# Optimization experiments

Measured on AMD Instinct MI355X. Metric: run time of the kernel, lower is better.

## Reference

```python
import jax, jax.numpy as jnp
import numpy as np

N, T, D, H, K = 2048, 128, 256, 256, 12
MAX_ITER = 100  # k-means max_iter from _cluster default


def setup_inputs() -> dict:
    key = jax.random.key(0)
    ks = jax.random.split(key, 16)
    std = 1.0 / np.sqrt(H).astype(np.float32)
    u = lambda k, shape: jax.random.uniform(k, shape, jnp.float32, -std, std)
    return {
        "x": jax.random.normal(ks[0], (N, T, D), jnp.float32),
        "lengths": jax.random.randint(ks[1], (N,), 1, T + 1),  # valid lens in [1, T]
        # GRU params (PyTorch layout: [3H, in], gate order r,z,n)
        "W_ih": u(ks[2], (3 * H, D)),
        "W_hh": u(ks[3], (3 * H, H)),
        "b_ih": u(ks[4], (3 * H,)),
        "b_hh": u(ks[5], (3 * H,)),
        # weight1 / weight2: nn.Linear(H, 1)
        "w1_w": u(ks[6], (1, H)), "w1_b": u(ks[7], (1,)),
        "w2_w": u(ks[8], (1, H)), "w2_b": u(ks[9], (1,)),
        # GCN layers: weight [H, H], bias [H]
        "g1_w": u(ks[10], (H, H)), "g1_b": u(ks[11], (H,)),
        "g2_w": u(ks[12], (H, H)), "g2_b": u(ks[13], (H,)),
    }


def _gru(x, W_ih, W_hh, b_ih, b_hh):
    # x: [N, T, D] -> outputs [T, N, H]
    def step(h, x_t):
        gx = x_t @ W_ih.T + b_ih          # [N, 3H]
        gh = h @ W_hh.T + b_hh            # [N, 3H]
        xr, xz, xn = jnp.split(gx, 3, axis=-1)
        hr, hz, hn = jnp.split(gh, 3, axis=-1)
        r = jax.nn.sigmoid(xr + hr)
        z = jax.nn.sigmoid(xz + hz)
        n = jnp.tanh(xn + r * hn)
        h_new = (1.0 - z) * n + z * h
        return h_new, h_new

    h0 = jnp.zeros((x.shape[0], W_hh.shape[1]), x.dtype)
    _, outs = jax.lax.scan(step, h0, jnp.swapaxes(x, 0, 1))
    return outs  # [T, N, H]


def _kmeans(data, k, max_iter=MAX_ITER):
    # data: [n, H]. Fixed-iteration Lloyd's: after convergence centers are a
    # fixed point, so running all max_iter iters matches the early-break loop.
    n = data.shape[0]
    idx = jax.random.permutation(jax.random.key(42), n)[:k]  # random init
    centers0 = data[idx]
    x2 = jnp.sum(data * data, axis=1, keepdims=True)  # [n, 1]

    def body(_, centers):
        # squared distances (same argmin as cdist)
        d2 = x2 - 2.0 * (data @ centers.T) + jnp.sum(centers * centers, axis=1)
        codes = jnp.argmin(d2, axis=1)  # [n]
        sums = jax.ops.segment_sum(data, codes, num_segments=k)       # [k, H]
        cnts = jax.ops.segment_sum(jnp.ones((n,), data.dtype), codes, num_segments=k)
        # empty clusters keep old center
        return jnp.where(cnts[:, None] > 0,
                         sums / jnp.maximum(cnts[:, None], 1.0),
                         centers)

    return jax.lax.fori_loop(0, max_iter, body, centers0)


def reference(x, lengths, W_ih, W_hh, b_ih, b_hh,
              w1_w, w1_b, w2_w, w2_b, g1_w, g1_b, g2_w, g2_b):
    outs = _gru(x, W_ih, W_hh, b_ih, b_hh)              # [T, N, H]
    n = x.shape[0]
    hidden_t = outs[lengths - 1, jnp.arange(n)]         # last valid step, [N, H]

    # clustering uses detached hidden states
    centers = _kmeans(jax.lax.stop_gradient(hidden_t), K)  # [K, H]

    e = jax.nn.relu(hidden_t @ centers.T)               # [N, K]
    scores = jax.nn.softmax(e, axis=-1)

    # adj = eye(K) so GraphConvolution reduces to an affine map
    h1 = jax.nn.relu(centers @ g1_w + g1_b)             # [K, H]
    h2 = jax.nn.relu(h1 @ g2_w + g2_b)                  # [K, H]

    clu_app = scores @ h2                               # [N, H]
    w1 = jax.nn.sigmoid(clu_app @ w1_w.T + w1_b)        # [N, 1]
    w2 = jax.nn.sigmoid(hidden_t @ w2_w.T + w2_b)       # [N, 1]
    w1n = w1 / (w1 + w2)
    return w1n * clu_app + (1.0 - w1n) * hidden_t       # [N, H]
```

## Files before the change

kernel.cpp:

```cpp
#include <hip/hip_runtime.h>
#include <cstdint>
#include <cstring>
#include <vector>
#include <algorithm>


namespace {
constexpr int Nn = 2048;
constexpr int Tt = 128;
constexpr int Dd = 256;
constexpr int Hh = 256;
constexpr int Kk = 12;
constexpr int MAXIT = 100;
}

struct IdxArgs { int v[Kk]; };

typedef float v2f __attribute__((ext_vector_type(2)));

__device__ __forceinline__ float sigm(float x) { return 1.0f / (1.0f + expf(-x)); }

#define PKFMA(A, X, W) \
  asm("v_pk_fma_f32 %0, %1, %2, %0" : "+v"(A) : "v"(X), "v"(W))
#define LO2(V) ((v2f){(V).x, (V).y})
#define HI2(V) ((v2f){(V).z, (V).w})

__global__ __launch_bounds__(64) void pack_w(
    const float* __restrict__ Wih, const float* __restrict__ Whh,
    float* __restrict__ pk)
{
  const int j = blockIdx.x;
  const int k4 = threadIdx.x;
  const int g = j >> 8, c = j & 255;
  float4 vih = *(const float4*)&Wih[(size_t)j * 256 + k4 * 4];
  float4 vhh = *(const float4*)&Whh[(size_t)j * 256 + k4 * 4];
  *(float4*)&pk[(((size_t)k4 * 6 + g) * 256 + c) * 4]       = vih;
  *(float4*)&pk[(((size_t)k4 * 6 + 3 + g) * 256 + c) * 4]   = vhh;
}

__global__ __launch_bounds__(512, 1) void gru_q(
    const float* __restrict__ x, const int* __restrict__ len,
    const float* __restrict__ pk,
    const float* __restrict__ bih, const float* __restrict__ bhh,
    float* __restrict__ hfin)
{
  __shared__ alignas(16) float xls[8][260];
  __shared__ alignas(16) float hls[8][260];
  __shared__ float4 pbuf[2][8][256];
  const int tid = threadIdx.x;
  const int cp = tid & 127;
  const int q  = tid >> 7;
  const int n0 = blockIdx.x * 8;
  const int C0 = cp, C1 = cp + 128;

  const float bir0 = bih[C0], bhr0 = bhh[C0];
  const float biz0 = bih[Hh + C0], bhz0 = bhh[Hh + C0];
  const float bin0 = bih[2 * Hh + C0], bhn0 = bhh[2 * Hh + C0];
  const float bir1 = bih[C1], bhr1 = bhh[C1];
  const float biz1 = bih[Hh + C1], bhz1 = bhh[Hh + C1];
  const float bin1 = bih[2 * Hh + C1], bhn1 = bhh[2 * Hh + C1];
  int L[8];
  #pragma unroll
  for (int r = 0; r < 8; ++r) L[r] = len[n0 + r];

  const int q16 = q * 16;
  const size_t cp4 = (size_t)cp * 4;

  if (tid < 256) {
    #pragma unroll
    for (int r = 0; r < 8; ++r) hls[r][tid] = 0.f;
  }

  for (int t = 0; t < Tt; ++t) {
    {
      int row = tid >> 6, c4 = tid & 63;
      *(float4*)&xls[row][c4 * 4] =
          *(const float4*)&x[(size_t)(n0 + row) * (Tt * Dd) + (size_t)t * Dd + c4 * 4];
    }
    __syncthreads();

    v2f aR[8][2] = {}, aZ[8][2] = {}, aXN[8][2] = {}, aHN[8][2] = {};

    #pragma unroll 1
    for (int i = 0; i < 16; ++i) {
      const int k4 = q16 + i;
      const float* pb = pk + (size_t)k4 * 6144 + cp4;
      float4 wr0 = *(const float4*)(pb);
      float4 wr1 = *(const float4*)(pb + 512);
      float4 wz0 = *(const float4*)(pb + 1024);
      float4 wz1 = *(const float4*)(pb + 1536);
      float4 wn0 = *(const float4*)(pb + 2048);
      float4 wn1 = *(const float4*)(pb + 2560);
      const int k = k4 * 4;
      #pragma unroll
      for (int r = 0; r < 8; ++r) {
        float4 xv = *(const float4*)&xls[r][k];
        v2f xlo = LO2(xv), xhi = HI2(xv);
        PKFMA(aR[r][0],  xlo, LO2(wr0)); PKFMA(aR[r][0],  xhi, HI2(wr0));
        PKFMA(aR[r][1],  xlo, LO2(wr1)); PKFMA(aR[r][1],  xhi, HI2(wr1));
        PKFMA(aZ[r][0],  xlo, LO2(wz0)); PKFMA(aZ[r][0],  xhi, HI2(wz0));
        PKFMA(aZ[r][1],  xlo, LO2(wz1)); PKFMA(aZ[r][1],  xhi, HI2(wz1));
        PKFMA(aXN[r][0], xlo, LO2(wn0)); PKFMA(aXN[r][0], xhi, HI2(wn0));
        PKFMA(aXN[r][1], xlo, LO2(wn1)); PKFMA(aXN[r][1], xhi, HI2(wn1));
      }
    }
    #pragma unroll 1
    for (int i = 0; i < 16; ++i) {
      const int k4 = q16 + i;
      const float* pb = pk + (size_t)k4 * 6144 + 3072 + cp4;
      float4 wr0 = *(const float4*)(pb);
      float4 wr1 = *(const float4*)(pb + 512);
      float4 wz0 = *(const float4*)(pb + 1024);
      float4 wz1 = *(const float4*)(pb + 1536);
      float4 wn0 = *(const float4*)(pb + 2048);
      float4 wn1 = *(const float4*)(pb + 2560);
      const int k = k4 * 4;
      #pragma unroll
      for (int r = 0; r < 8; ++r) {
        float4 hv = *(const float4*)&hls[r][k];
        v2f hlo = LO2(hv), hhi = HI2(hv);
        PKFMA(aR[r][0],  hlo, LO2(wr0)); PKFMA(aR[r][0],  hhi, HI2(wr0));
        PKFMA(aR[r][1],  hlo, LO2(wr1)); PKFMA(aR[r][1],  hhi, HI2(wr1));
        PKFMA(aZ[r][0],  hlo, LO2(wz0)); PKFMA(aZ[r][0],  hhi, HI2(wz0));
        PKFMA(aZ[r][1],  hlo, LO2(wz1)); PKFMA(aZ[r][1],  hhi, HI2(wz1));
        PKFMA(aHN[r][0], hlo, LO2(wn0)); PKFMA(aHN[r][0], hhi, HI2(wn0));
        PKFMA(aHN[r][1], hlo, LO2(wn1)); PKFMA(aHN[r][1], hhi, HI2(wn1));
      }
    }

    float fR[8][2], fZ[8][2], fX[8][2], fH[8][2];
    #pragma unroll
    for (int r = 0; r < 8; ++r) {
      fR[r][0] = aR[r][0].x + aR[r][0].y;  fR[r][1] = aR[r][1].x + aR[r][1].y;
      fZ[r][0] = aZ[r][0].x + aZ[r][0].y;  fZ[r][1] = aZ[r][1].x + aZ[r][1].y;
      fX[r][0] = aXN[r][0].x + aXN[r][0].y; fX[r][1] = aXN[r][1].x + aXN[r][1].y;
      fH[r][0] = aHN[r][0].x + aHN[r][0].y; fH[r][1] = aHN[r][1].x + aHN[r][1].y;
    }

    if (q == 1 || q == 3) {
      const int reg = q >> 1;
      #pragma unroll
      for (int r = 0; r < 8; ++r) {
        pbuf[reg][r][C0] = make_float4(fR[r][0], fZ[r][0], fX[r][0], fH[r][0]);
        pbuf[reg][r][C1] = make_float4(fR[r][1], fZ[r][1], fX[r][1], fH[r][1]);
      }
    }
    __syncthreads();
    if (q == 0 || q == 2) {
      const int reg = q >> 1;
      #pragma unroll
      for (int r = 0; r < 8; ++r) {
        float4 p0 = pbuf[reg][r][C0];
        float4 p1 = pbuf[reg][r][C1];
        fR[r][0] += p0.x; fZ[r][0] += p0.y; fX[r][0] += p0.z; fH[r][0] += p0.w;
        fR[r][1] += p1.x; fZ[r][1] += p1.y; fX[r][1] += p1.z; fH[r][1] += p1.w;
      }
    }
    __syncthreads();
    if (q == 2) {
      #pragma unroll
      for (int r = 0; r < 8; ++r) {
        pbuf[0][r][C0] = make_float4(fR[r][0], fZ[r][0], fX[r][0], fH[r][0]);
        pbuf[0][r][C1] = make_float4(fR[r][1], fZ[r][1], fX[r][1], fH[r][1]);
      }
    }
    __syncthreads();

    if (q == 0) {
      #pragma unroll
      for (int r = 0; r < 8; ++r) {
        if (t < L[r]) {
          float4 p0 = pbuf[0][r][C0];
          float4 p1 = pbuf[0][r][C1];
          float sR0 = fR[r][0] + p0.x, sZ0 = fZ[r][0] + p0.y;
          float sX0 = fX[r][0] + p0.z, sH0 = fH[r][0] + p0.w;
          float sR1 = fR[r][1] + p1.x, sZ1 = fZ[r][1] + p1.y;
          float sX1 = fX[r][1] + p1.z, sH1 = fH[r][1] + p1.w;
          float rg0 = sigm(sR0 + bir0 + bhr0);
          float zg0 = sigm(sZ0 + biz0 + bhz0);
          float ng0 = tanhf(sX0 + bin0 + rg0 * (sH0 + bhn0));
          float hv0 = (1.f - zg0) * ng0 + zg0 * hls[r][C0];
          float rg1 = sigm(sR1 + bir1 + bhr1);
          float zg1 = sigm(sZ1 + biz1 + bhz1);
          float ng1 = tanhf(sX1 + bin1 + rg1 * (sH1 + bhn1));
          float hv1 = (1.f - zg1) * ng1 + zg1 * hls[r][C1];
          hls[r][C0] = hv0;
          hls[r][C1] = hv1;
          if (t == L[r] - 1) {
            hfin[(size_t)(n0 + r) * Hh + C0] = hv0;
            hfin[(size_t)(n0 + r) * Hh + C1] = hv1;
          }
        }
      }
    }
    __syncthreads();
  }
}

__global__ void km_init(const float* __restrict__ dat, float* __restrict__ cent,
                        int* __restrict__ codes_prev, IdxArgs ia)
{
  int c = threadIdx.x;
  #pragma unroll
  for (int k = 0; k < Kk; ++k)
    cent[k * Hh + c] = dat[(size_t)ia.v[k] * Hh + c];
  #pragma unroll
  for (int i = 0; i < 8; ++i) codes_prev[i * 256 + c] = -1;
}

__global__ __launch_bounds__(256) void km_assign(
    const float* __restrict__ dat, const float* __restrict__ cent,
    float* __restrict__ part, int* __restrict__ pcnt,
    int* __restrict__ codes_prev, int* __restrict__ chg_it,
    const int* __restrict__ done)
{
  if (done[0]) return;
  __shared__ alignas(16) float cs[Kk][Hh];
  __shared__ alignas(16) float ps[4][Kk][Hh];
  __shared__ float c2s[Kk];
  __shared__ int pc[4][Kk];
  __shared__ int chg_l;
  const int tid = threadIdx.x;
  const int lane = tid & 63;
  const int w = tid >> 6;

  for (int i = tid; i < Kk * Hh; i += 256) ((float*)cs)[i] = cent[i];
  for (int i = tid; i < 4 * Kk * Hh; i += 256) ((float*)ps)[i] = 0.f;
  if (tid < 4 * Kk) ((int*)pc)[tid] = 0;
  if (tid == 0) chg_l = 0;
  __syncthreads();
  if (tid < Kk) {
    float s = 0.f;
    for (int c = 0; c < Hh; ++c) { float v = cs[tid][c]; s += v * v; }
    c2s[tid] = s;
  }
  __syncthreads();

  int mych = 0;
  const int base = blockIdx.x * 64 + w * 16;
  for (int rr = 0; rr < 16; ++rr) {
    const int n = base + rr;
    float4 v = *(const float4*)&dat[(size_t)n * Hh + lane * 4];
    float best = 3.4e38f; int bi = 0;
    #pragma unroll
    for (int k = 0; k < Kk; ++k) {
      float4 cv = *(const float4*)&cs[k][lane * 4];
      float p = v.x * cv.x + v.y * cv.y + v.z * cv.z + v.w * cv.w;
      #pragma unroll
      for (int m = 1; m < 64; m <<= 1) p += __shfl_xor(p, m, 64);
      float d = c2s[k] - 2.f * p;
      if (d < best) { best = d; bi = k; }
    }
    float4* dst = (float4*)&ps[w][bi][lane * 4];
    float4 cur = *dst;
    cur.x += v.x; cur.y += v.y; cur.z += v.z; cur.w += v.w;
    *dst = cur;
    if (lane == 0) {
      pc[w][bi] += 1;
      if (codes_prev[n] != bi) { codes_prev[n] = bi; mych = 1; }
    }
  }
  if (mych) atomicOr(&chg_l, 1);
  __syncthreads();
  const float* p0 = &ps[0][0][0];
  for (int i = tid; i < Kk * Hh; i += 256)
    part[(size_t)blockIdx.x * (Kk * Hh) + i] =
        p0[i] + p0[Kk * Hh + i] + p0[2 * Kk * Hh + i] + p0[3 * Kk * Hh + i];
  if (tid < Kk)
    pcnt[blockIdx.x * Kk + tid] = pc[0][tid] + pc[1][tid] + pc[2][tid] + pc[3][tid];
  if (tid == 0 && chg_l) atomicOr(chg_it, 1);
}

__global__ __launch_bounds__(256) void km_update(
    const float* __restrict__ part, const int* __restrict__ pcnt,
    float* __restrict__ cent, const int* __restrict__ chg_it,
    int* __restrict__ done)
{
  if (done[0]) return;
  int k = blockIdx.x, c = threadIdx.x;
  int cnt = 0;
  for (int p = 0; p < 32; ++p) cnt += pcnt[p * Kk + k];
  float s = 0.f;
  for (int p = 0; p < 32; ++p) s += part[(size_t)p * (Kk * Hh) + k * Hh + c];
  if (cnt > 0) cent[k * Hh + c] = s / (float)cnt;
  if (k == 0 && c == 0 && chg_it[0] == 0) done[0] = 1;
}

__global__ __launch_bounds__(256) void gcn(
    const float* __restrict__ cent, const float* __restrict__ g1w,
    const float* __restrict__ g1b, const float* __restrict__ g2w,
    const float* __restrict__ g2b, float* __restrict__ h2out)
{
  __shared__ float a[Kk][Hh];
  __shared__ float b[Kk][Hh];
  int c = threadIdx.x;
  for (int i = c; i < Kk * Hh; i += 256) ((float*)a)[i] = cent[i];
  __syncthreads();
  float acc[Kk];
  #pragma unroll
  for (int k = 0; k < Kk; ++k) acc[k] = 0.f;
  for (int j = 0; j < Hh; ++j) {
    float wv = g1w[(size_t)j * Hh + c];
    #pragma unroll
    for (int k = 0; k < Kk; ++k) acc[k] += a[k][j] * wv;
  }
  #pragma unroll
  for (int k = 0; k < Kk; ++k) b[k][c] = fmaxf(acc[k] + g1b[c], 0.f);
  __syncthreads();
  #pragma unroll
  for (int k = 0; k < Kk; ++k) acc[k] = 0.f;
  for (int j = 0; j < Hh; ++j) {
    float wv = g2w[(size_t)j * Hh + c];
    #pragma unroll
    for (int k = 0; k < Kk; ++k) acc[k] += b[k][j] * wv;
  }
  #pragma unroll
  for (int k = 0; k < Kk; ++k) h2out[k * Hh + c] = fmaxf(acc[k] + g2b[c], 0.f);
}

__global__ __launch_bounds__(256) void finalk(
    const float* __restrict__ hfin, const float* __restrict__ cent,
    const float* __restrict__ h2, const float* __restrict__ w1w,
    const float* __restrict__ w1b, const float* __restrict__ w2w,
    const float* __restrict__ w2b, float* __restrict__ out)
{
  __shared__ alignas(16) float cs[Kk][Hh];
  __shared__ alignas(16) float hs[Kk][Hh];
  __shared__ float red[4];
  const int tid = threadIdx.x, lane = tid & 63, w = tid >> 6;
  const int n = blockIdx.x;
  for (int i = tid; i < Kk * Hh; i += 256) { ((float*)cs)[i] = cent[i]; ((float*)hs)[i] = h2[i]; }
  float ht = hfin[(size_t)n * Hh + tid];
  __syncthreads();

  auto bred = [&](float v) -> float {
    #pragma unroll
    for (int m = 1; m < 64; m <<= 1) v += __shfl_xor(v, m, 64);
    __syncthreads();
    if (lane == 0) red[w] = v;
    __syncthreads();
    return red[0] + red[1] + red[2] + red[3];
  };

  float ev[Kk];
  #pragma unroll
  for (int k = 0; k < Kk; ++k)
    ev[k] = fmaxf(bred(ht * cs[k][tid]), 0.f);

  float mx = ev[0];
  #pragma unroll
  for (int k = 1; k < Kk; ++k) mx = fmaxf(mx, ev[k]);
  float se = 0.f; float sc[Kk];
  #pragma unroll
  for (int k = 0; k < Kk; ++k) { sc[k] = expf(ev[k] - mx); se += sc[k]; }
  float inv = 1.f / se;
  float clu = 0.f;
  #pragma unroll
  for (int k = 0; k < Kk; ++k) clu += sc[k] * inv * hs[k][tid];

  float r1 = bred(clu * w1w[tid]);
  float r2 = bred(ht * w2w[tid]);
  float a1 = sigm(r1 + w1b[0]);
  float a2 = sigm(r2 + w2b[0]);
  float wn = a1 / (a1 + a2);
  out[(size_t)n * Hh + tid] = wn * clu + (1.f - wn) * ht;
}

static void tf2x32(uint32_t k0, uint32_t k1, uint32_t c0, uint32_t c1,
                   uint32_t& o0, uint32_t& o1) {
  uint32_t ks2 = k0 ^ k1 ^ 0x1BD11BDAu;
  uint32_t x0 = c0 + k0, x1 = c1 + k1;
#define TFR(r) do { x0 += x1; x1 = (x1 << (r)) | (x1 >> (32 - (r))); x1 ^= x0; } while (0)
  TFR(13); TFR(15); TFR(26); TFR(6);
  x0 += k1;  x1 += ks2 + 1u;
  TFR(17); TFR(29); TFR(16); TFR(24);
  x0 += ks2; x1 += k0 + 2u;
  TFR(13); TFR(15); TFR(26); TFR(6);
  x0 += k0;  x1 += k1 + 3u;
  TFR(17); TFR(29); TFR(16); TFR(24);
  x0 += k1;  x1 += ks2 + 4u;
  TFR(13); TFR(15); TFR(26); TFR(6);
  x0 += ks2; x1 += k0 + 5u;
#undef TFR
  o0 = x0; o1 = x1;
}

static void compute_idx(int* out12) {
  uint32_t kh = 0u, kl = 42u;
  std::vector<int> perm(Nn);
  for (int i = 0; i < Nn; ++i) perm[i] = i;
  std::vector<uint32_t> bits(Nn);
  std::vector<int> pos(Nn);
  for (int round = 0; round < 2; ++round) {
    uint32_t nh, nl, sh, sl;
    tf2x32(kh, kl, 0u, 0u, nh, nl);
    tf2x32(kh, kl, 0u, 1u, sh, sl);
    kh = nh; kl = nl;
    for (uint32_t i = 0; i < (uint32_t)Nn; ++i) {
      uint32_t o0, o1; tf2x32(sh, sl, 0u, i, o0, o1); bits[i] = o0 ^ o1;
    }
    for (int i = 0; i < Nn; ++i) pos[i] = i;
    std::stable_sort(pos.begin(), pos.end(),
                     [&](int a, int b) { return bits[a] < bits[b]; });
    std::vector<int> np(Nn);
    for (int i = 0; i < Nn; ++i) np[i] = perm[pos[i]];
    perm.swap(np);
  }
  for (int k = 0; k < Kk; ++k) out12[k] = perm[k];
}

extern "C" void kernel_launch(void* const* d_in, const int* in_sizes, int n_in,
                              void* d_out, int out_size, void* d_ws, size_t ws_size,
                              hipStream_t stream) {
  const float* x   = (const float*)d_in[0];
  const int*   len = (const int*)d_in[1];
  const float* Wih = (const float*)d_in[2];
  const float* Whh = (const float*)d_in[3];
  const float* bih = (const float*)d_in[4];
  const float* bhh = (const float*)d_in[5];
  const float* w1w = (const float*)d_in[6];
  const float* w1b = (const float*)d_in[7];
  const float* w2w = (const float*)d_in[8];
  const float* w2b = (const float*)d_in[9];
  const float* g1w = (const float*)d_in[10];
  const float* g1b = (const float*)d_in[11];
  const float* g2w = (const float*)d_in[12];
  const float* g2b = (const float*)d_in[13];
  float* out = (float*)d_out;

  float* wsf  = (float*)d_ws;
  float* hfin = wsf;
  float* cent = hfin + (size_t)Nn * Hh;
  float* h2g  = cent + Kk * Hh;
  float* part = h2g + Kk * Hh;
  int*   pcnt = (int*)(part + 32 * Kk * Hh);
  int*   codes = pcnt + 512;
  int*   chg  = codes + Nn;
  float* pkw  = (float*)(chg + MAXIT + 28);

  IdxArgs ia;
  compute_idx(ia.v);

  hipMemsetAsync(chg, 0, (MAXIT + 1) * sizeof(int), stream);
  pack_w<<<768, 64, 0, stream>>>(Wih, Whh, pkw);
  gru_q<<<256, 512, 0, stream>>>(x, len, pkw, bih, bhh, hfin);

  int* done = chg + MAXIT;
  km_init<<<1, 256, 0, stream>>>(hfin, cent, codes, ia);
  for (int it = 0; it < MAXIT; ++it) {
    km_assign<<<32, 256, 0, stream>>>(hfin, cent, part, pcnt, codes, chg + it, done);
    km_update<<<Kk, 256, 0, stream>>>(part, pcnt, cent, chg + it, done);
  }

  gcn<<<1, 256, 0, stream>>>(cent, g1w, g1b, g2w, g2b, h2g);
  finalk<<<Nn, 256, 0, stream>>>(hfin, cent, h2g, w1w, w1b, w2w, w2b, out);
}
```

Measured before the change: 4.664 ms.

## Fuse k-means centroid update into assignment kernel with double-buffered partials

```diff
diff --git a/kernel.cpp b/kernel.cpp
--- a/kernel.cpp
+++ b/kernel.cpp
@@ -208,13 +208,18 @@
   for (int i = 0; i < 8; ++i) codes_prev[i * 256 + c] = -1;
 }
 
-__global__ __launch_bounds__(256) void km_assign(
-    const float* __restrict__ dat, const float* __restrict__ cent,
-    float* __restrict__ part, int* __restrict__ pcnt,
-    int* __restrict__ codes_prev, int* __restrict__ chg_it,
-    const int* __restrict__ done)
+__global__ __launch_bounds__(256) void km_step(
+    const float* __restrict__ dat, float* __restrict__ cent,
+    float* __restrict__ partA, float* __restrict__ partB,
+    int* __restrict__ pcntA, int* __restrict__ pcntB,
+    int* __restrict__ codes_prev, int* __restrict__ chg,
+    int* __restrict__ done, int it)
 {
   if (done[0]) return;
+  if (it > 0 && chg[it - 1] == 0) {
+    if (blockIdx.x == 0 && threadIdx.x == 0) done[0] = 1;
+    return;
+  }
   __shared__ alignas(16) float cs[Kk][Hh];
   __shared__ alignas(16) float ps[4][Kk][Hh];
   __shared__ float c2s[Kk];
@@ -223,12 +228,31 @@
   const int tid = threadIdx.x;
   const int lane = tid & 63;
   const int w = tid >> 6;
-
-  for (int i = tid; i < Kk * Hh; i += 256) ((float*)cs)[i] = cent[i];
+  float* pw = (it & 1) ? partB : partA;
+  const float* pr = (it & 1) ? partA : partB;
+  int* cw = (it & 1) ? pcntB : pcntA;
+  const int* cr = (it & 1) ? pcntA : pcntB;
+
+  if (it == 0) {
+    for (int i = tid; i < Kk * Hh; i += 256) ((float*)cs)[i] = cent[i];
+  } else {
+    const int c = tid;
+    #pragma unroll
+    for (int k = 0; k < Kk; ++k) {
+      int cnt = 0;
+      for (int p = 0; p < 32; ++p) cnt += cr[p * Kk + k];
+      float s = 0.f;
+      for (int p = 0; p < 32; ++p) s += pr[(size_t)p * (Kk * Hh) + k * Hh + c];
+      cs[k][c] = (cnt > 0) ? s / (float)cnt : cent[k * Hh + c];
+    }
+  }
   for (int i = tid; i < 4 * Kk * Hh; i += 256) ((float*)ps)[i] = 0.f;
   if (tid < 4 * Kk) ((int*)pc)[tid] = 0;
   if (tid == 0) chg_l = 0;
   __syncthreads();
+  if (it > 0 && blockIdx.x == 0) {
+    for (int i = tid; i < Kk * Hh; i += 256) cent[i] = ((const float*)cs)[i];
+  }
   if (tid < Kk) {
     float s = 0.f;
     for (int c = 0; c < Hh; ++c) { float v = cs[tid][c]; s += v * v; }
@@ -264,26 +288,24 @@
   __syncthreads();
   const float* p0 = &ps[0][0][0];
   for (int i = tid; i < Kk * Hh; i += 256)
-    part[(size_t)blockIdx.x * (Kk * Hh) + i] =
+    pw[(size_t)blockIdx.x * (Kk * Hh) + i] =
         p0[i] + p0[Kk * Hh + i] + p0[2 * Kk * Hh + i] + p0[3 * Kk * Hh + i];
   if (tid < Kk)
-    pcnt[blockIdx.x * Kk + tid] = pc[0][tid] + pc[1][tid] + pc[2][tid] + pc[3][tid];
-  if (tid == 0 && chg_l) atomicOr(chg_it, 1);
-}
-
-__global__ __launch_bounds__(256) void km_update(
-    const float* __restrict__ part, const int* __restrict__ pcnt,
-    float* __restrict__ cent, const int* __restrict__ chg_it,
-    int* __restrict__ done)
+    cw[blockIdx.x * Kk + tid] = pc[0][tid] + pc[1][tid] + pc[2][tid] + pc[3][tid];
+  if (tid == 0 && chg_l) atomicOr(chg + it, 1);
+}
+
+__global__ __launch_bounds__(256) void km_final(
+    const float* __restrict__ partB, const int* __restrict__ pcntB,
+    float* __restrict__ cent, const int* __restrict__ done)
 {
   if (done[0]) return;
   int k = blockIdx.x, c = threadIdx.x;
   int cnt = 0;
-  for (int p = 0; p < 32; ++p) cnt += pcnt[p * Kk + k];
+  for (int p = 0; p < 32; ++p) cnt += pcntB[p * Kk + k];
   float s = 0.f;
-  for (int p = 0; p < 32; ++p) s += part[(size_t)p * (Kk * Hh) + k * Hh + c];
+  for (int p = 0; p < 32; ++p) s += partB[(size_t)p * (Kk * Hh) + k * Hh + c];
   if (cnt > 0) cent[k * Hh + c] = s / (float)cnt;
-  if (k == 0 && c == 0 && chg_it[0] == 0) done[0] = 1;
 }
 
 __global__ __launch_bounds__(256) void gcn(
@@ -432,9 +454,11 @@
   float* hfin = wsf;
   float* cent = hfin + (size_t)Nn * Hh;
   float* h2g  = cent + Kk * Hh;
-  float* part = h2g + Kk * Hh;
-  int*   pcnt = (int*)(part + 32 * Kk * Hh);
-  int*   codes = pcnt + 512;
+  float* partA = h2g + Kk * Hh;
+  float* partB = partA + 32 * Kk * Hh;
+  int*   pcntA = (int*)(partB + 32 * Kk * Hh);
+  int*   pcntB = pcntA + 512;
+  int*   codes = pcntB + 512;
   int*   chg  = codes + Nn;
   float* pkw  = (float*)(chg + MAXIT + 28);
 
@@ -447,10 +471,10 @@
 
   int* done = chg + MAXIT;
   km_init<<<1, 256, 0, stream>>>(hfin, cent, codes, ia);
-  for (int it = 0; it < MAXIT; ++it) {
-    km_assign<<<32, 256, 0, stream>>>(hfin, cent, part, pcnt, codes, chg + it, done);
-    km_update<<<Kk, 256, 0, stream>>>(part, pcnt, cent, chg + it, done);
-  }
+  for (int it = 0; it < MAXIT; ++it)
+    km_step<<<32, 256, 0, stream>>>(hfin, cent, partA, partB, pcntA, pcntB,
+                                    codes, chg, done, it);
+  km_final<<<Kk, 256, 0, stream>>>(partB, pcntB, cent, done);
 
   gcn<<<1, 256, 0, stream>>>(cent, g1w, g1b, g2w, g2b, h2g);
   finalk<<<Nn, 256, 0, stream>>>(hfin, cent, h2g, w1w, w1b, w2w, w2b, out);
```

After: 4.760 ms. 2.0% more time.
